# Optimization experiments

Hardware: AMD Instinct MI355X
Metric: run time of the kernel (lower is better)

The kernel has to match this reference:

```python
import jax, jax.numpy as jnp
import numpy as np

H = 64   # hidden_dim
E = 5    # num_edge_features
F = 6    # num_node_features
B, W, N = 8, 12, 200
LN_EPS = 1e-5


def _lstm_layer(x, Wih, Whh, bih, bhh):
    # x: [BN, W, Fin] -> full output sequence [BN, W, H] (PyTorch gate order i,f,g,o)
    BN = x.shape[0]
    h0 = jnp.zeros((BN, Whh.shape[1]), x.dtype)
    def step(carry, xt):
        h, c = carry
        g = xt @ Wih.T + h @ Whh.T + (bih + bhh)
        i, f, gg, o = jnp.split(g, 4, axis=-1)
        c = jax.nn.sigmoid(f) * c + jax.nn.sigmoid(i) * jnp.tanh(gg)
        h = jax.nn.sigmoid(o) * jnp.tanh(c)
        return (h, c), h
    _, ys = jax.lax.scan(step, (h0, h0), jnp.swapaxes(x, 0, 1))
    return jnp.swapaxes(ys, 0, 1)


def _layernorm(x, g, b):
    mu = jnp.mean(x, axis=-1, keepdims=True)
    var = jnp.mean(jnp.square(x - mu), axis=-1, keepdims=True)
    return (x - mu) * jax.lax.rsqrt(var + LN_EPS) * g + b


def setup_inputs() -> dict:
    key = jax.random.key(0)
    ks = jax.random.split(key, 32)
    s = 0.05
    d = {
        'node_features': jax.random.normal(ks[0], (B, W, N, F), jnp.float32),
        'edge_features': jax.random.normal(ks[1], (B, W, N, N, E), jnp.float32),
        'adjacency': jax.random.uniform(ks[2], (B, N, N), jnp.float32),
        # LSTM layer 0 (input F) and layer 1 (input H)
        'Wih0': jax.random.normal(ks[3], (4 * H, F), jnp.float32) * s,
        'Whh0': jax.random.normal(ks[4], (4 * H, H), jnp.float32) * s,
        'bih0': jax.random.normal(ks[5], (4 * H,), jnp.float32) * s,
        'bhh0': jax.random.normal(ks[6], (4 * H,), jnp.float32) * s,
        'Wih1': jax.random.normal(ks[7], (4 * H, H), jnp.float32) * s,
        'Whh1': jax.random.normal(ks[8], (4 * H, H), jnp.float32) * s,
        'bih1': jax.random.normal(ks[9], (4 * H,), jnp.float32) * s,
        'bhh1': jax.random.normal(ks[10], (4 * H,), jnp.float32) * s,
        # 2 GCN layers: linear, edge projection, layernorm
        'gcn_W': jax.random.normal(ks[11], (2, H, H), jnp.float32) * s,
        'gcn_b': jax.random.normal(ks[12], (2, H), jnp.float32) * s,
        'ep_W': jax.random.normal(ks[13], (2, H, E), jnp.float32) * s,
        'ep_b': jax.random.normal(ks[14], (2, H), jnp.float32) * s,
        'ln_g': jnp.ones((2, H), jnp.float32),
        'ln_b': jnp.zeros((2, H), jnp.float32),
        # edge MLP: (2H+E) -> H -> H//2 -> 1
        'mlp_W1': jax.random.normal(ks[15], (H, 2 * H + E), jnp.float32) * s,
        'mlp_b1': jax.random.normal(ks[16], (H,), jnp.float32) * s,
        'mlp_W2': jax.random.normal(ks[17], (H // 2, H), jnp.float32) * s,
        'mlp_b2': jax.random.normal(ks[18], (H // 2,), jnp.float32) * s,
        'mlp_W3': jax.random.normal(ks[19], (1, H // 2), jnp.float32) * s,
        'mlp_b3': jax.random.normal(ks[20], (1,), jnp.float32) * s,
    }
    return d


def reference(node_features, edge_features, adjacency,
              Wih0, Whh0, bih0, bhh0, Wih1, Whh1, bih1, bhh1,
              gcn_W, gcn_b, ep_W, ep_b, ln_g, ln_b,
              mlp_W1, mlp_b1, mlp_W2, mlp_b2, mlp_W3, mlp_b3):
    Bn, Wn, Nn, _ = node_features.shape
    # [B,W,N,F] -> [B*N, W, F]
    x = jnp.transpose(node_features, (0, 2, 1, 3)).reshape(Bn * Nn, Wn, -1)
    y0 = _lstm_layer(x, Wih0, Whh0, bih0, bhh0)      # dropout between layers: eval mode (identity)
    y1 = _lstm_layer(y0, Wih1, Whh1, bih1, bhh1)
    h = y1[:, -1, :].reshape(Bn, Nn, H)

    edge_last = edge_features[:, -1]                 # [B,N,N,E]
    for i in range(2):
        edge_h = edge_last @ ep_W[i].T + ep_b[i]     # [B,N,N,H]
        messages = jnp.einsum('bij,bijn->bin', adjacency, edge_h)
        updated = h @ gcn_W[i].T + gcn_b[i] + messages
        h = jax.nn.relu(_layernorm(updated, ln_g[i], ln_b[i]))
        # dropout: eval mode (identity)

    h_i = jnp.broadcast_to(h[:, :, None, :], (Bn, Nn, Nn, H))
    h_j = jnp.broadcast_to(h[:, None, :, :], (Bn, Nn, Nn, H))
    edge_input = jnp.concatenate([h_i, h_j, edge_last], axis=-1)  # [B,N,N,2H+E]
    z = jax.nn.relu(edge_input @ mlp_W1.T + mlp_b1)
    z = jax.nn.relu(z @ mlp_W2.T + mlp_b2)
    logits = (z @ mlp_W3.T + mlp_b3)[..., 0]
    return jax.nn.sigmoid(logits)
```

## Files before the change

kernel.cpp:

```cpp
#include <hip/hip_runtime.h>
#include <math.h>


#define Hd   64
#define Ed   5
#define Fd   6
#define Bd   8
#define Wd   12
#define Nd   200
#define NSEQ (Bd*Nd)
#define NG   (4*Hd)
#define NEDGE (Bd*Nd*Nd)
#define LNEPS 1e-5f

__device__ __forceinline__ float sigm(float x) { return 1.0f / (1.0f + __expf(-x)); }
__device__ __forceinline__ float tanh_fast(float x) {
  float ax = fabsf(x);
  float t  = __expf(-2.0f * ax);
  float r  = (1.0f - t) / (1.0f + t);
  return copysignf(r, x);
}

__global__ __launch_bounds__(256) void k_prep(
    const float* __restrict__ Wih1, const float* __restrict__ gcn_W,
    const float* __restrict__ ep_W, const float* __restrict__ W1,
    float* __restrict__ Wt1, float* __restrict__ gcnWT,
    float* __restrict__ epWT, float* __restrict__ W1aT,
    float* __restrict__ W1bT)
{
  int idx = blockIdx.x * 256 + threadIdx.x;
  if (idx < 16384) {
    int k = idx >> 8, j = idx & 255;
    Wt1[idx] = Wih1[j * Hd + k];
  } else if (idx < 24576) {
    int r0 = idx - 16384;
    int round = r0 >> 12, rem = r0 & 4095;
    int k = rem >> 6, u = rem & 63;
    gcnWT[r0] = gcn_W[round * 4096 + u * 64 + k];
  } else if (idx < 25216) {
    int r0 = idx - 24576;
    int round = r0 / 320, rem = r0 % 320;
    int e = rem >> 6, u = rem & 63;
    epWT[r0] = ep_W[round * 320 + u * Ed + e];
  } else if (idx < 29312) {
    int r0 = idx - 25216;
    int k = r0 >> 6, n = r0 & 63;
    W1aT[r0] = W1[n * 133 + k];
  } else if (idx < 33408) {
    int r0 = idx - 29312;
    int k = r0 >> 6, n = r0 & 63;
    W1bT[r0] = W1[n * 133 + 64 + k];
  }
}

__global__ __launch_bounds__(256, 3) void k_lstm0(
    const float* __restrict__ nf,
    const float* __restrict__ Wih0, const float* __restrict__ Whh0,
    const float* __restrict__ bih0, const float* __restrict__ bhh0,
    float* __restrict__ y0)
{
  __shared__ float x_sh[Wd * Fd];
  __shared__ float h_sh[Hd];
  __shared__ float gate_sh[2][NG];

  const int tid = threadIdx.x;
  const int seq = blockIdx.x;
  const int b = seq / Nd, n = seq % Nd;
  const int u = tid & 63;

  if (tid < Wd * Fd) {
    int t = tid / Fd, f = tid % Fd;
    x_sh[tid] = nf[((b * Wd + t) * Nd + n) * Fd + f];
  }
  h_sh[u] = 0.f;

  const int j = tid;
  float4 wh[16];
  const float4* wrow = (const float4*)(Whh0 + j * Hd);
  #pragma unroll
  for (int q = 0; q < 16; ++q) wh[q] = wrow[q];
  float wx[Fd];
  #pragma unroll
  for (int f = 0; f < Fd; ++f) wx[f] = Wih0[j * Fd + f];
  const float bias = bih0[j] + bhh0[j];
  const int jt = j >> 6;

  float c = 0.f;
  float yreg[Wd];
  __syncthreads();

  for (int t = 0; t < Wd; ++t) {
    const float* xp = x_sh + t * Fd;
    float a0 = bias, a1 = 0.f, a2 = 0.f, a3 = 0.f;
    #pragma unroll
    for (int f = 0; f < Fd; ++f) a1 += xp[f] * wx[f];
    const float4* h4 = (const float4*)h_sh;
    #pragma unroll
    for (int q = 0; q < 16; ++q) {
      float4 hv = h4[q];
      float d = hv.x * wh[q].x + hv.y * wh[q].y + hv.z * wh[q].z + hv.w * wh[q].w;
      if ((q & 3) == 0) a0 += d; else if ((q & 3) == 1) a1 += d;
      else if ((q & 3) == 2) a2 += d; else a3 += d;
    }
    float acc = (a0 + a1) + (a2 + a3);
    gate_sh[t & 1][j] = (jt == 2) ? tanh_fast(acc) : sigm(acc);
    __syncthreads();
    const float* gb = gate_sh[t & 1];
    float iv = gb[u];
    float fv = gb[64 + u];
    float gv = gb[128 + u];
    float ov = gb[192 + u];
    c = fv * c + iv * gv;
    float h = ov * tanh_fast(c);
    h_sh[u] = h;
    yreg[t] = h;
  }
  if (tid < Hd) {
    #pragma unroll
    for (int t = 0; t < Wd; ++t)
      y0[seq * (Wd * Hd) + t * Hd + u] = yreg[t];
  }
}

__global__ __launch_bounds__(256) void k_xproj1(
    const float* __restrict__ y0,
    const float* __restrict__ Wt1,
    const float* __restrict__ bih1, const float* __restrict__ bhh1,
    float* __restrict__ G1)
{
  __shared__ float ysh[64 * 65];
  __shared__ float osh[2 * 64 * 65];

  const int tid  = threadIdx.x;
  const int row0 = blockIdx.x * 64;
  for (int idx = tid; idx < 64 * 64; idx += 256) {
    int r = idx >> 6, k = idx & 63;
    ysh[r * 65 + k] = y0[(row0 + r) * Hd + k];
  }
  __syncthreads();

  const int w = __builtin_amdgcn_readfirstlane(tid >> 6);
  const int r = tid & 63;
  float acc[64];
  #pragma unroll
  for (int c = 0; c < 64; ++c) acc[c] = 0.f;

  const float* wbase = Wt1 + (w << 6);
  #pragma unroll 2
  for (int k = 0; k < 64; ++k) {
    float yv = ysh[r * 65 + k];
    const float* wk = wbase + k * NG;
    #pragma unroll
    for (int c = 0; c < 64; ++c) acc[c] = fmaf(yv, wk[c], acc[c]);
  }
  #pragma unroll
  for (int c = 0; c < 64; ++c) acc[c] += bih1[(w << 6) + c] + bhh1[(w << 6) + c];

  #pragma unroll
  for (int p = 0; p < 2; ++p) {
    __syncthreads();
    if ((w >> 1) == p) {
      float* orow = osh + ((w & 1) * 64 + r) * 65;
      #pragma unroll
      for (int c = 0; c < 64; ++c) orow[c] = acc[c];
    }
    __syncthreads();
    for (int idx = tid; idx < 2 * 64 * 64; idx += 256) {
      int c  = idx & 127;
      int rr = idx >> 7;
      G1[(row0 + rr) * NG + p * 128 + c] =
          osh[((c >> 6) * 64 + rr) * 65 + (c & 63)];
    }
  }
}

__global__ __launch_bounds__(256, 3) void k_lstm1(
    const float* __restrict__ G1,
    const float* __restrict__ Whh1,
    float* __restrict__ hout)
{
  __shared__ float h_sh[Hd];
  __shared__ float gate_sh[2][NG];

  const int tid = threadIdx.x;
  const int seq = blockIdx.x;
  const int u = tid & 63;
  h_sh[u] = 0.f;

  const int j = tid;
  float4 wh[16];
  const float4* wrow = (const float4*)(Whh1 + j * Hd);
  #pragma unroll
  for (int q = 0; q < 16; ++q) wh[q] = wrow[q];
  const int jt = j >> 6;
  float c = 0.f;
  float hlast = 0.f;

  float g_cur = G1[(seq * Wd + 0) * NG + j];
  __syncthreads();

  for (int t = 0; t < Wd; ++t) {
    float g_next = (t + 1 < Wd) ? G1[(seq * Wd + t + 1) * NG + j] : 0.f;
    float a0 = g_cur;
    float a1 = 0.f, a2 = 0.f, a3 = 0.f;
    const float4* h4 = (const float4*)h_sh;
    #pragma unroll
    for (int q = 0; q < 16; ++q) {
      float4 hv = h4[q];
      float d = hv.x * wh[q].x + hv.y * wh[q].y + hv.z * wh[q].z + hv.w * wh[q].w;
      if ((q & 3) == 0) a0 += d; else if ((q & 3) == 1) a1 += d;
      else if ((q & 3) == 2) a2 += d; else a3 += d;
    }
    float acc = (a0 + a1) + (a2 + a3);
    gate_sh[t & 1][j] = (jt == 2) ? tanh_fast(acc) : sigm(acc);
    __syncthreads();
    const float* gb = gate_sh[t & 1];
    float iv = gb[u];
    float fv = gb[64 + u];
    float gv = gb[128 + u];
    float ov = gb[192 + u];
    c = fv * c + iv * gv;
    float h = ov * tanh_fast(c);
    h_sh[u] = h;
    hlast = h;
    g_cur = g_next;
  }
  if (tid < Hd) hout[seq * Hd + u] = hlast;
}

__global__ __launch_bounds__(256) void k_node(
    const float* __restrict__ ef,    const float* __restrict__ adj,
    const float* __restrict__ h0,
    const float* __restrict__ gcnWT, const float* __restrict__ gcn_b,
    const float* __restrict__ epWT,  const float* __restrict__ ep_b,
    const float* __restrict__ ln_g,  const float* __restrict__ ln_b,
    const float* __restrict__ W1aT,  const float* __restrict__ W1bT,
    const float* __restrict__ b1,
    float* __restrict__ uu, float* __restrict__ vt)
{
  __shared__ float ef_sh[Nd * Ed];
  __shared__ float adj_sh[Nd];
  __shared__ float red[4][6];
  __shared__ float w6[6];
  __shared__ float hcur[Hd];

  const int row = blockIdx.x;
  const int b = row / Nd, i = row % Nd;
  const int tid = threadIdx.x;

  const float* efrow = ef + (size_t)(((b * Wd + (Wd - 1)) * Nd + i)) * (Nd * Ed);
  for (int idx = tid; idx < Nd * Ed; idx += 256) ef_sh[idx] = efrow[idx];
  const float* adjrow = adj + (b * Nd + i) * Nd;
  if (tid < Nd) adj_sh[tid] = adjrow[tid];
  if (tid < Hd) hcur[tid] = h0[row * Hd + tid];
  __syncthreads();

  float p[6] = {0.f, 0.f, 0.f, 0.f, 0.f, 0.f};
  if (tid < Nd) {
    float a = adj_sh[tid];
    p[5] = a;
    #pragma unroll
    for (int k = 0; k < Ed; ++k) p[k] = a * ef_sh[tid * Ed + k];
  }
  #pragma unroll
  for (int k = 0; k < 6; ++k) {
    float v = p[k];
    for (int off = 32; off > 0; off >>= 1) v += __shfl_down(v, off);
    p[k] = v;
  }
  if ((tid & 63) == 0) {
    #pragma unroll
    for (int k = 0; k < 6; ++k) red[tid >> 6][k] = p[k];
  }
  __syncthreads();
  if (tid < 6)
    w6[tid] = red[0][tid] + red[1][tid] + red[2][tid] + red[3][tid];
  __syncthreads();

  const int u = tid & 63;
  #pragma unroll
  for (int round = 0; round < 2; ++round) {
    float hnew = 0.f;
    if (tid < 64) {
      const float* gwT = gcnWT + round * 4096;
      const float* ewT = epWT  + round * 320;
      float acc = gcn_b[round * Hd + u] + w6[5] * ep_b[round * Hd + u];
      #pragma unroll
      for (int e = 0; e < Ed; ++e) acc += w6[e] * ewT[e * 64 + u];
      #pragma unroll 8
      for (int k = 0; k < Hd; ++k) acc += hcur[k] * gwT[k * 64 + u];

      float mu = acc;
      #pragma unroll
      for (int off = 1; off < 64; off <<= 1) mu += __shfl_xor(mu, off);
      mu *= (1.f / 64.f);
      float d = acc - mu;
      float var = d * d;
      #pragma unroll
      for (int off = 1; off < 64; off <<= 1) var += __shfl_xor(var, off);
      var *= (1.f / 64.f);
      float v = d * rsqrtf(var + LNEPS) * ln_g[round * Hd + u] + ln_b[round * Hd + u];
      hnew = fmaxf(v, 0.f);
    }
    __syncthreads();
    if (tid < 64) hcur[tid] = hnew;
    __syncthreads();
  }

  if (tid < 64) {
    float acc = b1[tid];
    #pragma unroll 8
    for (int k = 0; k < Hd; ++k) acc += hcur[k] * W1aT[k * 64 + tid];
    uu[row * Hd + tid] = acc;
  } else if (tid < 128) {
    const int n = tid - 64;
    float acc = 0.f;
    #pragma unroll 8
    for (int k = 0; k < Hd; ++k) acc += hcur[k] * W1bT[k * 64 + n];
    vt[n * NSEQ + row] = acc;
  }
}

__global__ __launch_bounds__(256) void k_mlp(
    const float* __restrict__ ef,
    const float* __restrict__ u, const float* __restrict__ vt,
    const float* __restrict__ W1,
    const float* __restrict__ W2, const float* __restrict__ b2,
    const float* __restrict__ W3, const float* __restrict__ b3,
    float* __restrict__ out)
{
  const int idx = blockIdx.x * 256 + threadIdx.x;
  const int b   = idx / (Nd * Nd);
  const int rem = idx - b * Nd * Nd;
  const int i   = rem / Nd;
  const int jj  = rem - i * Nd;

  const float* e = ef + (((b * Wd + (Wd - 1)) * Nd + i) * Nd + jj) * Ed;
  float e5[Ed];
  #pragma unroll
  for (int q = 0; q < Ed; ++q) e5[q] = e[q];

  const float* ur = u + (b * Nd + i) * Hd;
  const int vcol = b * Nd + jj;

  float z1[64];
  #pragma unroll
  for (int k = 0; k < 64; ++k) {
    float acc = ur[k] + vt[k * NSEQ + vcol];
    const float* w1c = W1 + k * 133 + 128;
    #pragma unroll
    for (int q = 0; q < Ed; ++q) acc += e5[q] * w1c[q];
    z1[k] = fmaxf(acc, 0.f);
  }

  float logit = b3[0];
  #pragma unroll 4
  for (int o = 0; o < 32; ++o) {
    float a0 = b2[o], a1 = 0.f, a2 = 0.f, a3 = 0.f;
    const float* w2 = W2 + o * 64;
    #pragma unroll
    for (int k = 0; k < 64; k += 4) {
      a0 += w2[k]     * z1[k];
      a1 += w2[k + 1] * z1[k + 1];
      a2 += w2[k + 2] * z1[k + 2];
      a3 += w2[k + 3] * z1[k + 3];
    }
    float z2 = fmaxf((a0 + a1) + (a2 + a3), 0.f);
    logit += W3[o] * z2;
  }
  out[idx] = 1.f / (1.f + __expf(-logit));
}

extern "C" void kernel_launch(void* const* d_in, const int* in_sizes, int n_in,
                              void* d_out, int out_size, void* d_ws, size_t ws_size,
                              hipStream_t stream) {
  (void)in_sizes; (void)n_in; (void)out_size; (void)ws_size;
  const float* nf   = (const float*)d_in[0];
  const float* ef   = (const float*)d_in[1];
  const float* adj  = (const float*)d_in[2];
  const float* Wih0 = (const float*)d_in[3];
  const float* Whh0 = (const float*)d_in[4];
  const float* bih0 = (const float*)d_in[5];
  const float* bhh0 = (const float*)d_in[6];
  const float* Wih1 = (const float*)d_in[7];
  const float* Whh1 = (const float*)d_in[8];
  const float* bih1 = (const float*)d_in[9];
  const float* bhh1 = (const float*)d_in[10];
  const float* gcnW = (const float*)d_in[11];
  const float* gcnB = (const float*)d_in[12];
  const float* epW  = (const float*)d_in[13];
  const float* epB  = (const float*)d_in[14];
  const float* lnG  = (const float*)d_in[15];
  const float* lnB  = (const float*)d_in[16];
  const float* W1   = (const float*)d_in[17];
  const float* b1   = (const float*)d_in[18];
  const float* W2   = (const float*)d_in[19];
  const float* b2   = (const float*)d_in[20];
  const float* W3   = (const float*)d_in[21];
  const float* b3   = (const float*)d_in[22];
  float* out = (float*)d_out;

  float* ws   = (float*)d_ws;
  float* y0   = ws;
  float* G1   = y0   + 1228800;
  float* Wt1  = G1   + 4915200;
  float* h0   = Wt1  + 16384;
  float* uu   = h0   + 102400;
  float* vt   = uu   + 102400;
  float* gWT  = vt   + 102400;
  float* eWT  = gWT  + 8192;
  float* W1aT = eWT  + 640;
  float* W1bT = W1aT + 4096;

  k_prep  <<<131,  256, 0, stream>>>(Wih1, gcnW, epW, W1,
                                     Wt1, gWT, eWT, W1aT, W1bT);
  k_lstm0 <<<NSEQ, 256, 0, stream>>>(nf, Wih0, Whh0, bih0, bhh0, y0);
  k_xproj1<<<300,  256, 0, stream>>>(y0, Wt1, bih1, bhh1, G1);
  k_lstm1 <<<NSEQ, 256, 0, stream>>>(G1, Whh1, h0);
  k_node  <<<1600, 256, 0, stream>>>(ef, adj, h0, gWT, gcnB, eWT, epB,
                                     lnG, lnB, W1aT, W1bT, b1, uu, vt);
  k_mlp   <<<1250, 256, 0, stream>>>(ef, uu, vt, W1, W2, b2, W3, b3, out);
}
```

Baseline: 270.2 us.

## Batch four LSTM sequences per block with shared-memory recurrent weights

Replaces the per-sequence LSTM kernels with one generic kernel that processes four sequences per block. The transposed recurrent weights are staged mostly in LDS, with a small tail kept in registers, and each weight load is reused across the four sequences. Layer-0 input projection becomes a separate precompute pass into a G0 buffer, so both layers share the same kernel. This trades an extra 19.6 MB gate buffer write and read, plus a second barrier per step, for less weight traffic and four times fewer blocks.

```diff
diff --git a/kernel.cpp b/kernel.cpp
--- a/kernel.cpp
+++ b/kernel.cpp
@@ -11,6 +11,8 @@
 #define NSEQ (Bd*Nd)
 #define NG   (4*Hd)
 #define NEDGE (Bd*Nd*Nd)
+#define SEQB 4
+#define WROWS 58
 #define LNEPS 1e-5f
 
 __device__ __forceinline__ float sigm(float x) { return 1.0f / (1.0f + __expf(-x)); }
@@ -24,9 +26,14 @@
 __global__ __launch_bounds__(256) void k_prep(
     const float* __restrict__ Wih1, const float* __restrict__ gcn_W,
     const float* __restrict__ ep_W, const float* __restrict__ W1,
+    const float* __restrict__ Wih0, const float* __restrict__ bih0,
+    const float* __restrict__ bhh0, const float* __restrict__ Whh0,
+    const float* __restrict__ Whh1,
     float* __restrict__ Wt1, float* __restrict__ gcnWT,
     float* __restrict__ epWT, float* __restrict__ W1aT,
-    float* __restrict__ W1bT)
+    float* __restrict__ W1bT, float* __restrict__ Wt0,
+    float* __restrict__ b0s, float* __restrict__ WhhT0,
+    float* __restrict__ WhhT1)
 {
   int idx = blockIdx.x * 256 + threadIdx.x;
   if (idx < 16384) {
@@ -50,75 +57,132 @@
     int r0 = idx - 29312;
     int k = r0 >> 6, n = r0 & 63;
     W1bT[r0] = W1[n * 133 + 64 + k];
-  }
-}
-
-__global__ __launch_bounds__(256, 3) void k_lstm0(
-    const float* __restrict__ nf,
-    const float* __restrict__ Wih0, const float* __restrict__ Whh0,
-    const float* __restrict__ bih0, const float* __restrict__ bhh0,
-    float* __restrict__ y0)
-{
-  __shared__ float x_sh[Wd * Fd];
-  __shared__ float h_sh[Hd];
-  __shared__ float gate_sh[2][NG];
-
-  const int tid = threadIdx.x;
-  const int seq = blockIdx.x;
-  const int b = seq / Nd, n = seq % Nd;
-  const int u = tid & 63;
-
-  if (tid < Wd * Fd) {
-    int t = tid / Fd, f = tid % Fd;
-    x_sh[tid] = nf[((b * Wd + t) * Nd + n) * Fd + f];
-  }
-  h_sh[u] = 0.f;
-
-  const int j = tid;
-  float4 wh[16];
-  const float4* wrow = (const float4*)(Whh0 + j * Hd);
-  #pragma unroll
-  for (int q = 0; q < 16; ++q) wh[q] = wrow[q];
-  float wx[Fd];
-  #pragma unroll
-  for (int f = 0; f < Fd; ++f) wx[f] = Wih0[j * Fd + f];
-  const float bias = bih0[j] + bhh0[j];
+  } else if (idx < 34944) {
+    int r0 = idx - 33408;
+    int f = r0 >> 8, j = r0 & 255;
+    Wt0[r0] = Wih0[j * Fd + f];
+  } else if (idx < 35200) {
+    int j = idx - 34944;
+    b0s[j] = bih0[j] + bhh0[j];
+  } else if (idx < 51584) {
+    int r0 = idx - 35200;
+    int k = r0 >> 8, j = r0 & 255;
+    WhhT0[r0] = Whh0[j * Hd + k];
+  } else if (idx < 67968) {
+    int r0 = idx - 51584;
+    int k = r0 >> 8, j = r0 & 255;
+    WhhT1[r0] = Whh1[j * Hd + k];
+  }
+}
+
+__global__ __launch_bounds__(256) void k_xproj0(
+    const float* __restrict__ nf, const float* __restrict__ Wt0,
+    const float* __restrict__ b0s, float* __restrict__ G0)
+{
+  const int j = threadIdx.x;
+  const int row0 = blockIdx.x * 8;
+  float wcol[Fd];
+  #pragma unroll
+  for (int f = 0; f < Fd; ++f) wcol[f] = Wt0[f * NG + j];
+  const float bj = b0s[j];
+  #pragma unroll
+  for (int r = 0; r < 8; ++r) {
+    int row = row0 + r;
+    int seq = row / Wd, t = row % Wd;
+    int b = seq / Nd, n = seq % Nd;
+    const float* xp = nf + ((b * Wd + t) * Nd + n) * Fd;
+    float acc = bj;
+    #pragma unroll
+    for (int f = 0; f < Fd; ++f) acc += xp[f] * wcol[f];
+    G0[row * NG + j] = acc;
+  }
+}
+
+__global__ __launch_bounds__(256, 2) void k_lstm(
+    const float* __restrict__ G,
+    const float* __restrict__ WhhT,
+    float* __restrict__ yfull,
+    float* __restrict__ hlast,
+    int store_all)
+{
+  __shared__ float w_lds[WROWS * NG];
+  __shared__ float h_sh[SEQB][Hd];
+  __shared__ float gate_sh[SEQB][NG];
+
+  const int tid  = threadIdx.x;
+  const int seq0 = blockIdx.x * SEQB;
+  const int j    = tid;
+  const int su   = tid >> 6;
+  const int uu   = tid & 63;
+
+  for (int idx = tid; idx < WROWS * NG; idx += 256) w_lds[idx] = WhhT[idx];
+  float wtail[Hd - WROWS];
+  #pragma unroll
+  for (int q = 0; q < Hd - WROWS; ++q) wtail[q] = WhhT[(WROWS + q) * NG + j];
+  h_sh[su][uu] = 0.f;
+
   const int jt = j >> 6;
-
   float c = 0.f;
   float yreg[Wd];
+  float hl = 0.f;
+
+  float gc[SEQB];
+  #pragma unroll
+  for (int s = 0; s < SEQB; ++s) gc[s] = G[((seq0 + s) * Wd + 0) * NG + j];
   __syncthreads();
 
+#define WK(k) ((k) < WROWS ? w_lds[(k) * NG + j] : wtail[(k) - WROWS])
+
   for (int t = 0; t < Wd; ++t) {
-    const float* xp = x_sh + t * Fd;
-    float a0 = bias, a1 = 0.f, a2 = 0.f, a3 = 0.f;
-    #pragma unroll
-    for (int f = 0; f < Fd; ++f) a1 += xp[f] * wx[f];
-    const float4* h4 = (const float4*)h_sh;
+    float gn[SEQB];
+    #pragma unroll
+    for (int s = 0; s < SEQB; ++s)
+      gn[s] = (t + 1 < Wd) ? G[((seq0 + s) * Wd + t + 1) * NG + j] : 0.f;
+
+    float a[SEQB][4];
+    #pragma unroll
+    for (int s = 0; s < SEQB; ++s) {
+      a[s][0] = gc[s]; a[s][1] = 0.f; a[s][2] = 0.f; a[s][3] = 0.f;
+    }
     #pragma unroll
     for (int q = 0; q < 16; ++q) {
-      float4 hv = h4[q];
-      float d = hv.x * wh[q].x + hv.y * wh[q].y + hv.z * wh[q].z + hv.w * wh[q].w;
-      if ((q & 3) == 0) a0 += d; else if ((q & 3) == 1) a1 += d;
-      else if ((q & 3) == 2) a2 += d; else a3 += d;
-    }
-    float acc = (a0 + a1) + (a2 + a3);
-    gate_sh[t & 1][j] = (jt == 2) ? tanh_fast(acc) : sigm(acc);
-    __syncthreads();
-    const float* gb = gate_sh[t & 1];
-    float iv = gb[u];
-    float fv = gb[64 + u];
-    float gv = gb[128 + u];
-    float ov = gb[192 + u];
-    c = fv * c + iv * gv;
-    float h = ov * tanh_fast(c);
-    h_sh[u] = h;
-    yreg[t] = h;
-  }
-  if (tid < Hd) {
+      float w0 = WK(4 * q), w1 = WK(4 * q + 1);
+      float w2 = WK(4 * q + 2), w3 = WK(4 * q + 3);
+      #pragma unroll
+      for (int s = 0; s < SEQB; ++s) {
+        float4 hv = ((const float4*)h_sh[s])[q];
+        a[s][q & 3] += hv.x * w0 + hv.y * w1 + hv.z * w2 + hv.w * w3;
+      }
+    }
+    #pragma unroll
+    for (int s = 0; s < SEQB; ++s) {
+      float acc = (a[s][0] + a[s][1]) + (a[s][2] + a[s][3]);
+      gate_sh[s][j] = (jt == 2) ? tanh_fast(acc) : sigm(acc);
+    }
+    __syncthreads();
+    {
+      float iv = gate_sh[su][uu];
+      float fv = gate_sh[su][64 + uu];
+      float gv = gate_sh[su][128 + uu];
+      float ov = gate_sh[su][192 + uu];
+      c = fv * c + iv * gv;
+      float h = ov * tanh_fast(c);
+      h_sh[su][uu] = h;
+      yreg[t] = h;
+      hl = h;
+    }
+    __syncthreads();
+    #pragma unroll
+    for (int s = 0; s < SEQB; ++s) gc[s] = gn[s];
+  }
+#undef WK
+
+  if (store_all) {
     #pragma unroll
     for (int t = 0; t < Wd; ++t)
-      y0[seq * (Wd * Hd) + t * Hd + u] = yreg[t];
+      yfull[(seq0 + su) * (Wd * Hd) + t * Hd + uu] = yreg[t];
+  } else {
+    hlast[(seq0 + su) * Hd + uu] = hl;
   }
 }
 
@@ -172,60 +236,6 @@
           osh[((c >> 6) * 64 + rr) * 65 + (c & 63)];
     }
   }
-}
-
-__global__ __launch_bounds__(256, 3) void k_lstm1(
-    const float* __restrict__ G1,
-    const float* __restrict__ Whh1,
-    float* __restrict__ hout)
-{
-  __shared__ float h_sh[Hd];
-  __shared__ float gate_sh[2][NG];
-
-  const int tid = threadIdx.x;
-  const int seq = blockIdx.x;
-  const int u = tid & 63;
-  h_sh[u] = 0.f;
-
-  const int j = tid;
-  float4 wh[16];
-  const float4* wrow = (const float4*)(Whh1 + j * Hd);
-  #pragma unroll
-  for (int q = 0; q < 16; ++q) wh[q] = wrow[q];
-  const int jt = j >> 6;
-  float c = 0.f;
-  float hlast = 0.f;
-
-  float g_cur = G1[(seq * Wd + 0) * NG + j];
-  __syncthreads();
-
-  for (int t = 0; t < Wd; ++t) {
-    float g_next = (t + 1 < Wd) ? G1[(seq * Wd + t + 1) * NG + j] : 0.f;
-    float a0 = g_cur;
-    float a1 = 0.f, a2 = 0.f, a3 = 0.f;
-    const float4* h4 = (const float4*)h_sh;
-    #pragma unroll
-    for (int q = 0; q < 16; ++q) {
-      float4 hv = h4[q];
-      float d = hv.x * wh[q].x + hv.y * wh[q].y + hv.z * wh[q].z + hv.w * wh[q].w;
-      if ((q & 3) == 0) a0 += d; else if ((q & 3) == 1) a1 += d;
-      else if ((q & 3) == 2) a2 += d; else a3 += d;
-    }
-    float acc = (a0 + a1) + (a2 + a3);
-    gate_sh[t & 1][j] = (jt == 2) ? tanh_fast(acc) : sigm(acc);
-    __syncthreads();
-    const float* gb = gate_sh[t & 1];
-    float iv = gb[u];
-    float fv = gb[64 + u];
-    float gv = gb[128 + u];
-    float ov = gb[192 + u];
-    c = fv * c + iv * gv;
-    float h = ov * tanh_fast(c);
-    h_sh[u] = h;
-    hlast = h;
-    g_cur = g_next;
-  }
-  if (tid < Hd) hout[seq * Hd + u] = hlast;
 }
 
 __global__ __launch_bounds__(256) void k_node(
@@ -400,23 +410,30 @@
   const float* b3   = (const float*)d_in[22];
   float* out = (float*)d_out;
 
-  float* ws   = (float*)d_ws;
-  float* y0   = ws;
-  float* G1   = y0   + 1228800;
-  float* Wt1  = G1   + 4915200;
-  float* h0   = Wt1  + 16384;
-  float* uu   = h0   + 102400;
-  float* vt   = uu   + 102400;
-  float* gWT  = vt   + 102400;
-  float* eWT  = gWT  + 8192;
-  float* W1aT = eWT  + 640;
-  float* W1bT = W1aT + 4096;
-
-  k_prep  <<<131,  256, 0, stream>>>(Wih1, gcnW, epW, W1,
-                                     Wt1, gWT, eWT, W1aT, W1bT);
-  k_lstm0 <<<NSEQ, 256, 0, stream>>>(nf, Wih0, Whh0, bih0, bhh0, y0);
+  float* ws    = (float*)d_ws;
+  float* y0    = ws;
+  float* G1    = y0    + 1228800;
+  float* G0    = G1    + 4915200;
+  float* Wt1   = G0    + 4915200;
+  float* h0    = Wt1   + 16384;
+  float* uu    = h0    + 102400;
+  float* vt    = uu    + 102400;
+  float* gWT   = vt    + 102400;
+  float* eWT   = gWT   + 8192;
+  float* W1aT  = eWT   + 640;
+  float* W1bT  = W1aT  + 4096;
+  float* Wt0   = W1bT  + 4096;
+  float* b0s   = Wt0   + 1536;
+  float* WhhT0 = b0s   + 256;
+  float* WhhT1 = WhhT0 + 16384;
+
+  k_prep  <<<266,  256, 0, stream>>>(Wih1, gcnW, epW, W1, Wih0, bih0, bhh0,
+                                     Whh0, Whh1, Wt1, gWT, eWT, W1aT, W1bT,
+                                     Wt0, b0s, WhhT0, WhhT1);
+  k_xproj0<<<2400, 256, 0, stream>>>(nf, Wt0, b0s, G0);
+  k_lstm  <<<NSEQ/SEQB, 256, 0, stream>>>(G0, WhhT0, y0, h0, 1);
   k_xproj1<<<300,  256, 0, stream>>>(y0, Wt1, bih1, bhh1, G1);
-  k_lstm1 <<<NSEQ, 256, 0, stream>>>(G1, Whh1, h0);
+  k_lstm  <<<NSEQ/SEQB, 256, 0, stream>>>(G1, WhhT1, y0, h0, 0);
   k_node  <<<1600, 256, 0, stream>>>(ef, adj, h0, gWT, gcnB, eWT, epB,
                                      lnG, lnB, W1aT, W1bT, b1, uu, vt);
   k_mlp   <<<1250, 256, 0, stream>>>(ef, uu, vt, W1, W2, b2, W3, b3, out);
```

New measurement: 372.9 us. 38.0% more time.

## Fuse layer-1 input projection into LSTM1 and stage recurrent weights in LDS

Applied to the files above, without the earlier changes.

Removes the separate k_xproj1 kernel and its large G1 intermediate buffer by computing each sequence's layer-1 input gates inside k_lstm1 from y0 held in shared memory. Both LSTM kernels now keep most of the transposed recurrent weight matrix (58 of 64 rows) in LDS, plus a small per-thread register tail, instead of 64 floats per thread in registers. The launch-bounds occupancy hint is dropped. The aim is to cut global traffic and register pressure. The cost is about 60KB of LDS per block, which limits blocks per CU, and every block re-reads the weights from global memory.

```diff
diff --git a/kernel.cpp b/kernel.cpp
--- a/kernel.cpp
+++ b/kernel.cpp
@@ -11,6 +11,7 @@
 #define NSEQ (Bd*Nd)
 #define NG   (4*Hd)
 #define NEDGE (Bd*Nd*Nd)
+#define WROWS 58
 #define LNEPS 1e-5f
 
 __device__ __forceinline__ float sigm(float x) { return 1.0f / (1.0f + __expf(-x)); }
@@ -24,9 +25,11 @@
 __global__ __launch_bounds__(256) void k_prep(
     const float* __restrict__ Wih1, const float* __restrict__ gcn_W,
     const float* __restrict__ ep_W, const float* __restrict__ W1,
+    const float* __restrict__ Whh0, const float* __restrict__ Whh1,
     float* __restrict__ Wt1, float* __restrict__ gcnWT,
     float* __restrict__ epWT, float* __restrict__ W1aT,
-    float* __restrict__ W1bT)
+    float* __restrict__ W1bT, float* __restrict__ WhhT0,
+    float* __restrict__ WhhT1)
 {
   int idx = blockIdx.x * 256 + threadIdx.x;
   if (idx < 16384) {
@@ -50,35 +53,46 @@
     int r0 = idx - 29312;
     int k = r0 >> 6, n = r0 & 63;
     W1bT[r0] = W1[n * 133 + 64 + k];
-  }
-}
-
-__global__ __launch_bounds__(256, 3) void k_lstm0(
+  } else if (idx < 49792) {
+    int r0 = idx - 33408;
+    int k = r0 >> 8, j = r0 & 255;
+    WhhT0[r0] = Whh0[j * Hd + k];
+  } else if (idx < 66176) {
+    int r0 = idx - 49792;
+    int k = r0 >> 8, j = r0 & 255;
+    WhhT1[r0] = Whh1[j * Hd + k];
+  }
+}
+
+#define WK(k) ((k) < WROWS ? w_lds[(k) * NG + j] : wtail[(k) - WROWS])
+
+__global__ __launch_bounds__(256) void k_lstm0(
     const float* __restrict__ nf,
-    const float* __restrict__ Wih0, const float* __restrict__ Whh0,
-    const float* __restrict__ bih0, const float* __restrict__ bhh0,
+    const float* __restrict__ Wih0, const float* __restrict__ bih0,
+    const float* __restrict__ bhh0, const float* __restrict__ WhhT0,
     float* __restrict__ y0)
 {
+  __shared__ float w_lds[WROWS * NG];
+  __shared__ float gate_sh[2][NG];
+  __shared__ float h_sh[Hd];
   __shared__ float x_sh[Wd * Fd];
-  __shared__ float h_sh[Hd];
-  __shared__ float gate_sh[2][NG];
 
   const int tid = threadIdx.x;
   const int seq = blockIdx.x;
   const int b = seq / Nd, n = seq % Nd;
   const int u = tid & 63;
-
+  const int j = tid;
+
+  for (int idx = tid; idx < WROWS * NG; idx += 256) w_lds[idx] = WhhT0[idx];
+  float wtail[Hd - WROWS];
+  #pragma unroll
+  for (int q = 0; q < Hd - WROWS; ++q) wtail[q] = WhhT0[(WROWS + q) * NG + j];
   if (tid < Wd * Fd) {
     int t = tid / Fd, f = tid % Fd;
     x_sh[tid] = nf[((b * Wd + t) * Nd + n) * Fd + f];
   }
   h_sh[u] = 0.f;
 
-  const int j = tid;
-  float4 wh[16];
-  const float4* wrow = (const float4*)(Whh0 + j * Hd);
-  #pragma unroll
-  for (int q = 0; q < 16; ++q) wh[q] = wrow[q];
   float wx[Fd];
   #pragma unroll
   for (int f = 0; f < Fd; ++f) wx[f] = Wih0[j * Fd + f];
@@ -89,6 +103,7 @@
   float yreg[Wd];
   __syncthreads();
 
+  #pragma unroll
   for (int t = 0; t < Wd; ++t) {
     const float* xp = x_sh + t * Fd;
     float a0 = bias, a1 = 0.f, a2 = 0.f, a3 = 0.f;
@@ -98,7 +113,9 @@
     #pragma unroll
     for (int q = 0; q < 16; ++q) {
       float4 hv = h4[q];
-      float d = hv.x * wh[q].x + hv.y * wh[q].y + hv.z * wh[q].z + hv.w * wh[q].w;
+      float w0 = WK(4 * q),     w1 = WK(4 * q + 1);
+      float w2 = WK(4 * q + 2), w3 = WK(4 * q + 3);
+      float d = hv.x * w0 + hv.y * w1 + hv.z * w2 + hv.w * w3;
       if ((q & 3) == 0) a0 += d; else if ((q & 3) == 1) a1 += d;
       else if ((q & 3) == 2) a2 += d; else a3 += d;
     }
@@ -122,92 +139,60 @@
   }
 }
 
-__global__ __launch_bounds__(256) void k_xproj1(
+__global__ __launch_bounds__(256) void k_lstm1(
     const float* __restrict__ y0,
     const float* __restrict__ Wt1,
     const float* __restrict__ bih1, const float* __restrict__ bhh1,
-    float* __restrict__ G1)
-{
-  __shared__ float ysh[64 * 65];
-  __shared__ float osh[2 * 64 * 65];
-
-  const int tid  = threadIdx.x;
-  const int row0 = blockIdx.x * 64;
-  for (int idx = tid; idx < 64 * 64; idx += 256) {
-    int r = idx >> 6, k = idx & 63;
-    ysh[r * 65 + k] = y0[(row0 + r) * Hd + k];
-  }
-  __syncthreads();
-
-  const int w = __builtin_amdgcn_readfirstlane(tid >> 6);
-  const int r = tid & 63;
-  float acc[64];
-  #pragma unroll
-  for (int c = 0; c < 64; ++c) acc[c] = 0.f;
-
-  const float* wbase = Wt1 + (w << 6);
-  #pragma unroll 2
-  for (int k = 0; k < 64; ++k) {
-    float yv = ysh[r * 65 + k];
-    const float* wk = wbase + k * NG;
-    #pragma unroll
-    for (int c = 0; c < 64; ++c) acc[c] = fmaf(yv, wk[c], acc[c]);
-  }
-  #pragma unroll
-  for (int c = 0; c < 64; ++c) acc[c] += bih1[(w << 6) + c] + bhh1[(w << 6) + c];
-
-  #pragma unroll
-  for (int p = 0; p < 2; ++p) {
-    __syncthreads();
-    if ((w >> 1) == p) {
-      float* orow = osh + ((w & 1) * 64 + r) * 65;
-      #pragma unroll
-      for (int c = 0; c < 64; ++c) orow[c] = acc[c];
-    }
-    __syncthreads();
-    for (int idx = tid; idx < 2 * 64 * 64; idx += 256) {
-      int c  = idx & 127;
-      int rr = idx >> 7;
-      G1[(row0 + rr) * NG + p * 128 + c] =
-          osh[((c >> 6) * 64 + rr) * 65 + (c & 63)];
-    }
-  }
-}
-
-__global__ __launch_bounds__(256, 3) void k_lstm1(
-    const float* __restrict__ G1,
-    const float* __restrict__ Whh1,
+    const float* __restrict__ WhhT1,
     float* __restrict__ hout)
 {
+  __shared__ float w_lds[WROWS * NG];
+  __shared__ float gate_sh[2][NG];
   __shared__ float h_sh[Hd];
-  __shared__ float gate_sh[2][NG];
+  __shared__ float y0sh[Wd * Hd];
 
   const int tid = threadIdx.x;
   const int seq = blockIdx.x;
   const int u = tid & 63;
+  const int j = tid;
+
+  for (int idx = tid; idx < WROWS * NG; idx += 256) w_lds[idx] = WhhT1[idx];
+  float wtail[Hd - WROWS];
+  #pragma unroll
+  for (int q = 0; q < Hd - WROWS; ++q) wtail[q] = WhhT1[(WROWS + q) * NG + j];
+  for (int idx = tid; idx < Wd * Hd; idx += 256)
+    y0sh[idx] = y0[seq * (Wd * Hd) + idx];
   h_sh[u] = 0.f;
-
-  const int j = tid;
-  float4 wh[16];
-  const float4* wrow = (const float4*)(Whh1 + j * Hd);
-  #pragma unroll
-  for (int q = 0; q < 16; ++q) wh[q] = wrow[q];
+  __syncthreads();
+
+  float g[Wd];
+  #pragma unroll
+  for (int t = 0; t < Wd; ++t) g[t] = 0.f;
+  for (int k = 0; k < Hd; ++k) {
+    float wv = Wt1[k * NG + j];
+    #pragma unroll
+    for (int t = 0; t < Wd; ++t)
+      g[t] = fmaf(y0sh[t * Hd + k], wv, g[t]);
+  }
+  const float bsum = bih1[j] + bhh1[j];
+  #pragma unroll
+  for (int t = 0; t < Wd; ++t) g[t] += bsum;
+
   const int jt = j >> 6;
   float c = 0.f;
   float hlast = 0.f;
 
-  float g_cur = G1[(seq * Wd + 0) * NG + j];
-  __syncthreads();
-
+  #pragma unroll
   for (int t = 0; t < Wd; ++t) {
-    float g_next = (t + 1 < Wd) ? G1[(seq * Wd + t + 1) * NG + j] : 0.f;
-    float a0 = g_cur;
+    float a0 = g[t];
     float a1 = 0.f, a2 = 0.f, a3 = 0.f;
     const float4* h4 = (const float4*)h_sh;
     #pragma unroll
     for (int q = 0; q < 16; ++q) {
       float4 hv = h4[q];
-      float d = hv.x * wh[q].x + hv.y * wh[q].y + hv.z * wh[q].z + hv.w * wh[q].w;
+      float w0 = WK(4 * q),     w1 = WK(4 * q + 1);
+      float w2 = WK(4 * q + 2), w3 = WK(4 * q + 3);
+      float d = hv.x * w0 + hv.y * w1 + hv.z * w2 + hv.w * w3;
       if ((q & 3) == 0) a0 += d; else if ((q & 3) == 1) a1 += d;
       else if ((q & 3) == 2) a2 += d; else a3 += d;
     }
@@ -223,7 +208,6 @@
     float h = ov * tanh_fast(c);
     h_sh[u] = h;
     hlast = h;
-    g_cur = g_next;
   }
   if (tid < Hd) hout[seq * Hd + u] = hlast;
 }
@@ -400,23 +384,23 @@
   const float* b3   = (const float*)d_in[22];
   float* out = (float*)d_out;
 
-  float* ws   = (float*)d_ws;
-  float* y0   = ws;
-  float* G1   = y0   + 1228800;
-  float* Wt1  = G1   + 4915200;
-  float* h0   = Wt1  + 16384;
-  float* uu   = h0   + 102400;
-  float* vt   = uu   + 102400;
-  float* gWT  = vt   + 102400;
-  float* eWT  = gWT  + 8192;
-  float* W1aT = eWT  + 640;
-  float* W1bT = W1aT + 4096;
-
-  k_prep  <<<131,  256, 0, stream>>>(Wih1, gcnW, epW, W1,
-                                     Wt1, gWT, eWT, W1aT, W1bT);
-  k_lstm0 <<<NSEQ, 256, 0, stream>>>(nf, Wih0, Whh0, bih0, bhh0, y0);
-  k_xproj1<<<300,  256, 0, stream>>>(y0, Wt1, bih1, bhh1, G1);
-  k_lstm1 <<<NSEQ, 256, 0, stream>>>(G1, Whh1, h0);
+  float* ws    = (float*)d_ws;
+  float* y0    = ws;
+  float* Wt1   = y0    + 1228800;
+  float* h0    = Wt1   + 16384;
+  float* uu    = h0    + 102400;
+  float* vt    = uu    + 102400;
+  float* gWT   = vt    + 102400;
+  float* eWT   = gWT   + 8192;
+  float* W1aT  = eWT   + 640;
+  float* W1bT  = W1aT  + 4096;
+  float* WhhT0 = W1bT  + 4096;
+  float* WhhT1 = WhhT0 + 16384;
+
+  k_prep  <<<259,  256, 0, stream>>>(Wih1, gcnW, epW, W1, Whh0, Whh1,
+                                     Wt1, gWT, eWT, W1aT, W1bT, WhhT0, WhhT1);
+  k_lstm0 <<<NSEQ, 256, 0, stream>>>(nf, Wih0, bih0, bhh0, WhhT0, y0);
+  k_lstm1 <<<NSEQ, 256, 0, stream>>>(y0, Wt1, bih1, bhh1, WhhT1, h0);
   k_node  <<<1600, 256, 0, stream>>>(ef, adj, h0, gWT, gcnB, eWT, epB,
                                      lnG, lnB, W1aT, W1bT, b1, uu, vt);
   k_mlp   <<<1250, 256, 0, stream>>>(ef, uu, vt, W1, W2, b2, W3, b3, out);
```

After: 304.7 us. +12.8%, slower.

## Process two LSTM sequences per block with LDS weights and readlane broadcast

Applied to the files above, without the earlier changes.

Both LSTM recurrence kernels now handle two sequences per block. The recurrent weight matrix is staged once into padded LDS, where before each thread kept its row in registers. The hidden state is broadcast with readlane from the first wavefront's registers instead of an LDS h buffer, and k_lstm0 writes its outputs through an LDS staging buffer. The goal is to halve the block count, amortize weight loading, and add independent work per sync. In exchange each block uses about 80KB of LDS, occupancy drops to 2 blocks per CU, and every inner-loop step reads weights from LDS.

```diff
diff --git a/kernel.cpp b/kernel.cpp
--- a/kernel.cpp
+++ b/kernel.cpp
@@ -11,6 +11,7 @@
 #define NSEQ (Bd*Nd)
 #define NG   (4*Hd)
 #define NEDGE (Bd*Nd*Nd)
+#define WSTRIDE 68
 #define LNEPS 1e-5f
 
 __device__ __forceinline__ float sigm(float x) { return 1.0f / (1.0f + __expf(-x)); }
@@ -20,13 +21,18 @@
   float r  = (1.0f - t) / (1.0f + t);
   return copysignf(r, x);
 }
+__device__ __forceinline__ float rlane(float v, int lane) {
+  return __uint_as_float(__builtin_amdgcn_readlane(__float_as_uint(v), lane));
+}
 
 __global__ __launch_bounds__(256) void k_prep(
     const float* __restrict__ Wih1, const float* __restrict__ gcn_W,
     const float* __restrict__ ep_W, const float* __restrict__ W1,
+    const float* __restrict__ Whh0, const float* __restrict__ Whh1,
     float* __restrict__ Wt1, float* __restrict__ gcnWT,
     float* __restrict__ epWT, float* __restrict__ W1aT,
-    float* __restrict__ W1bT)
+    float* __restrict__ W1bT, float* __restrict__ Whh0P,
+    float* __restrict__ Whh1P)
 {
   int idx = blockIdx.x * 256 + threadIdx.x;
   if (idx < 16384) {
@@ -50,75 +56,101 @@
     int r0 = idx - 29312;
     int k = r0 >> 6, n = r0 & 63;
     W1bT[r0] = W1[n * 133 + 64 + k];
-  }
-}
-
-__global__ __launch_bounds__(256, 3) void k_lstm0(
+  } else if (idx < 50816) {
+    int r0 = idx - 33408;
+    int j = r0 / WSTRIDE, k = r0 % WSTRIDE;
+    Whh0P[r0] = (k < Hd) ? Whh0[j * Hd + k] : 0.f;
+  } else if (idx < 68224) {
+    int r0 = idx - 50816;
+    int j = r0 / WSTRIDE, k = r0 % WSTRIDE;
+    Whh1P[r0] = (k < Hd) ? Whh1[j * Hd + k] : 0.f;
+  }
+}
+
+__global__ __launch_bounds__(256, 2) void k_lstm0(
     const float* __restrict__ nf,
-    const float* __restrict__ Wih0, const float* __restrict__ Whh0,
-    const float* __restrict__ bih0, const float* __restrict__ bhh0,
+    const float* __restrict__ Wih0, const float* __restrict__ bih0,
+    const float* __restrict__ bhh0, const float* __restrict__ Whh0P,
     float* __restrict__ y0)
 {
-  __shared__ float x_sh[Wd * Fd];
-  __shared__ float h_sh[Hd];
-  __shared__ float gate_sh[2][NG];
-
-  const int tid = threadIdx.x;
-  const int seq = blockIdx.x;
-  const int b = seq / Nd, n = seq % Nd;
+  extern __shared__ float smem[];
+  float* w_lds = smem;
+  float* gates = smem + 17408;
+  float* x_sh  = gates + 1024;
+  float* y_sh  = x_sh + 144;
+
+  const int tid  = threadIdx.x;
+  const int seq0 = blockIdx.x * 2;
+  const int j = tid;
   const int u = tid & 63;
 
-  if (tid < Wd * Fd) {
-    int t = tid / Fd, f = tid % Fd;
-    x_sh[tid] = nf[((b * Wd + t) * Nd + n) * Fd + f];
-  }
-  h_sh[u] = 0.f;
-
-  const int j = tid;
-  float4 wh[16];
-  const float4* wrow = (const float4*)(Whh0 + j * Hd);
-  #pragma unroll
-  for (int q = 0; q < 16; ++q) wh[q] = wrow[q];
+  {
+    const float4* wsrc = (const float4*)Whh0P;
+    float4* wdst = (float4*)w_lds;
+    for (int idx = tid; idx < 4352; idx += 256) wdst[idx] = wsrc[idx];
+  }
+  for (int idx = tid; idx < 2 * Wd * Fd; idx += 256) {
+    int s = idx / (Wd * Fd); int rem = idx % (Wd * Fd);
+    int t = rem / Fd;        int f   = rem % Fd;
+    int seq = seq0 + s; int b = seq / Nd; int n = seq % Nd;
+    x_sh[idx] = nf[((b * Wd + t) * Nd + n) * Fd + f];
+  }
+
   float wx[Fd];
   #pragma unroll
   for (int f = 0; f < Fd; ++f) wx[f] = Wih0[j * Fd + f];
   const float bias = bih0[j] + bhh0[j];
   const int jt = j >> 6;
 
-  float c = 0.f;
-  float yreg[Wd];
-  __syncthreads();
+  float h0v = 0.f, h1v = 0.f, c0 = 0.f, c1 = 0.f;
+  __syncthreads();
+
+  const float4* w4p = (const float4*)w_lds + j * (WSTRIDE / 4);
 
   for (int t = 0; t < Wd; ++t) {
-    const float* xp = x_sh + t * Fd;
-    float a0 = bias, a1 = 0.f, a2 = 0.f, a3 = 0.f;
-    #pragma unroll
-    for (int f = 0; f < Fd; ++f) a1 += xp[f] * wx[f];
-    const float4* h4 = (const float4*)h_sh;
+    const float* xp0 = x_sh + (0 * Wd + t) * Fd;
+    const float* xp1 = x_sh + (1 * Wd + t) * Fd;
+    float as0[4] = {bias, 0.f, 0.f, 0.f};
+    float as1[4] = {bias, 0.f, 0.f, 0.f};
+    #pragma unroll
+    for (int f = 0; f < Fd; ++f) as0[1] += xp0[f] * wx[f];
+    #pragma unroll
+    for (int f = 0; f < Fd; ++f) as1[1] += xp1[f] * wx[f];
     #pragma unroll
     for (int q = 0; q < 16; ++q) {
-      float4 hv = h4[q];
-      float d = hv.x * wh[q].x + hv.y * wh[q].y + hv.z * wh[q].z + hv.w * wh[q].w;
-      if ((q & 3) == 0) a0 += d; else if ((q & 3) == 1) a1 += d;
-      else if ((q & 3) == 2) a2 += d; else a3 += d;
-    }
-    float acc = (a0 + a1) + (a2 + a3);
-    gate_sh[t & 1][j] = (jt == 2) ? tanh_fast(acc) : sigm(acc);
-    __syncthreads();
-    const float* gb = gate_sh[t & 1];
-    float iv = gb[u];
-    float fv = gb[64 + u];
-    float gv = gb[128 + u];
-    float ov = gb[192 + u];
-    c = fv * c + iv * gv;
-    float h = ov * tanh_fast(c);
-    h_sh[u] = h;
-    yreg[t] = h;
-  }
-  if (tid < Hd) {
-    #pragma unroll
-    for (int t = 0; t < Wd; ++t)
-      y0[seq * (Wd * Hd) + t * Hd + u] = yreg[t];
+      float4 w4 = w4p[q];
+      float d0 = rlane(h0v, 4 * q)     * w4.x + rlane(h0v, 4 * q + 1) * w4.y +
+                 rlane(h0v, 4 * q + 2) * w4.z + rlane(h0v, 4 * q + 3) * w4.w;
+      float d1 = rlane(h1v, 4 * q)     * w4.x + rlane(h1v, 4 * q + 1) * w4.y +
+                 rlane(h1v, 4 * q + 2) * w4.z + rlane(h1v, 4 * q + 3) * w4.w;
+      as0[q & 3] += d0;
+      as1[q & 3] += d1;
+    }
+    float acc0 = (as0[0] + as0[1]) + (as0[2] + as0[3]);
+    float acc1 = (as1[0] + as1[1]) + (as1[2] + as1[3]);
+    gates[(t & 1) * 512 + j]       = (jt == 2) ? tanh_fast(acc0) : sigm(acc0);
+    gates[(t & 1) * 512 + 256 + j] = (jt == 2) ? tanh_fast(acc1) : sigm(acc1);
+    __syncthreads();
+    const float* gb = gates + (t & 1) * 512;
+    {
+      float iv = gb[u], fv = gb[64 + u], gv = gb[128 + u], ov = gb[192 + u];
+      c0 = fv * c0 + iv * gv;
+      h0v = ov * tanh_fast(c0);
+    }
+    {
+      float iv = gb[256 + u], fv = gb[320 + u], gv = gb[384 + u], ov = gb[448 + u];
+      c1 = fv * c1 + iv * gv;
+      h1v = ov * tanh_fast(c1);
+    }
+    if (tid < Hd) {
+      y_sh[(0 * Wd + t) * 64 + u] = h0v;
+      y_sh[(1 * Wd + t) * 64 + u] = h1v;
+    }
+  }
+  __syncthreads();
+  for (int idx = tid; idx < 2 * Wd * Hd; idx += 256) {
+    int s = idx / (Wd * Hd), rem = idx % (Wd * Hd);
+    y0[(seq0 + s) * (Wd * Hd) + rem] = y_sh[idx];
   }
 }
 
@@ -174,58 +206,71 @@
   }
 }
 
-__global__ __launch_bounds__(256, 3) void k_lstm1(
+__global__ __launch_bounds__(256, 2) void k_lstm1(
     const float* __restrict__ G1,
-    const float* __restrict__ Whh1,
+    const float* __restrict__ Whh1P,
     float* __restrict__ hout)
 {
-  __shared__ float h_sh[Hd];
-  __shared__ float gate_sh[2][NG];
-
-  const int tid = threadIdx.x;
-  const int seq = blockIdx.x;
+  extern __shared__ float smem[];
+  float* w_lds = smem;
+  float* gates = smem + 17408;
+
+  const int tid  = threadIdx.x;
+  const int seq0 = blockIdx.x * 2;
+  const int j = tid;
   const int u = tid & 63;
-  h_sh[u] = 0.f;
-
-  const int j = tid;
-  float4 wh[16];
-  const float4* wrow = (const float4*)(Whh1 + j * Hd);
-  #pragma unroll
-  for (int q = 0; q < 16; ++q) wh[q] = wrow[q];
+
+  {
+    const float4* wsrc = (const float4*)Whh1P;
+    float4* wdst = (float4*)w_lds;
+    for (int idx = tid; idx < 4352; idx += 256) wdst[idx] = wsrc[idx];
+  }
   const int jt = j >> 6;
-  float c = 0.f;
-  float hlast = 0.f;
-
-  float g_cur = G1[(seq * Wd + 0) * NG + j];
-  __syncthreads();
+  float h0v = 0.f, h1v = 0.f, c0 = 0.f, c1 = 0.f;
+  float gc0 = G1[((seq0 + 0) * Wd + 0) * NG + j];
+  float gc1 = G1[((seq0 + 1) * Wd + 0) * NG + j];
+  __syncthreads();
+
+  const float4* w4p = (const float4*)w_lds + j * (WSTRIDE / 4);
 
   for (int t = 0; t < Wd; ++t) {
-    float g_next = (t + 1 < Wd) ? G1[(seq * Wd + t + 1) * NG + j] : 0.f;
-    float a0 = g_cur;
-    float a1 = 0.f, a2 = 0.f, a3 = 0.f;
-    const float4* h4 = (const float4*)h_sh;
+    float gn0 = (t + 1 < Wd) ? G1[((seq0 + 0) * Wd + t + 1) * NG + j] : 0.f;
+    float gn1 = (t + 1 < Wd) ? G1[((seq0 + 1) * Wd + t + 1) * NG + j] : 0.f;
+    float as0[4] = {gc0, 0.f, 0.f, 0.f};
+    float as1[4] = {gc1, 0.f, 0.f, 0.f};
     #pragma unroll
     for (int q = 0; q < 16; ++q) {
-      float4 hv = h4[q];
-      float d = hv.x * wh[q].x + hv.y * wh[q].y + hv.z * wh[q].z + hv.w * wh[q].w;
-      if ((q & 3) == 0) a0 += d; else if ((q & 3) == 1) a1 += d;
-      else if ((q & 3) == 2) a2 += d; else a3 += d;
-    }
-    float acc = (a0 + a1) + (a2 + a3);
-    gate_sh[t & 1][j] = (jt == 2) ? tanh_fast(acc) : sigm(acc);
-    __syncthreads();
-    const float* gb = gate_sh[t & 1];
-    float iv = gb[u];
-    float fv = gb[64 + u];
-    float gv = gb[128 + u];
-    float ov = gb[192 + u];
-    c = fv * c + iv * gv;
-    float h = ov * tanh_fast(c);
-    h_sh[u] = h;
-    hlast = h;
-    g_cur = g_next;
-  }
-  if (tid < Hd) hout[seq * Hd + u] = hlast;
+      float4 w4 = w4p[q];
+      float d0 = rlane(h0v, 4 * q)     * w4.x + rlane(h0v, 4 * q + 1) * w4.y +
+                 rlane(h0v, 4 * q + 2) * w4.z + rlane(h0v, 4 * q + 3) * w4.w;
+      float d1 = rlane(h1v, 4 * q)     * w4.x + rlane(h1v, 4 * q + 1) * w4.y +
+                 rlane(h1v, 4 * q + 2) * w4.z + rlane(h1v, 4 * q + 3) * w4.w;
+      as0[q & 3] += d0;
+      as1[q & 3] += d1;
+    }
+    float acc0 = (as0[0] + as0[1]) + (as0[2] + as0[3]);
+    float acc1 = (as1[0] + as1[1]) + (as1[2] + as1[3]);
+    gates[(t & 1) * 512 + j]       = (jt == 2) ? tanh_fast(acc0) : sigm(acc0);
+    gates[(t & 1) * 512 + 256 + j] = (jt == 2) ? tanh_fast(acc1) : sigm(acc1);
+    __syncthreads();
+    const float* gb = gates + (t & 1) * 512;
+    {
+      float iv = gb[u], fv = gb[64 + u], gv = gb[128 + u], ov = gb[192 + u];
+      c0 = fv * c0 + iv * gv;
+      h0v = ov * tanh_fast(c0);
+    }
+    {
+      float iv = gb[256 + u], fv = gb[320 + u], gv = gb[384 + u], ov = gb[448 + u];
+      c1 = fv * c1 + iv * gv;
+      h1v = ov * tanh_fast(c1);
+    }
+    gc0 = gn0;
+    gc1 = gn1;
+  }
+  if (tid < 128) {
+    int s = tid >> 6;
+    hout[(seq0 + s) * Hd + u] = (s == 0) ? h0v : h1v;
+  }
 }
 
 __global__ __launch_bounds__(256) void k_node(
@@ -400,23 +445,32 @@
   const float* b3   = (const float*)d_in[22];
   float* out = (float*)d_out;
 
-  float* ws   = (float*)d_ws;
-  float* y0   = ws;
-  float* G1   = y0   + 1228800;
-  float* Wt1  = G1   + 4915200;
-  float* h0   = Wt1  + 16384;
-  float* uu   = h0   + 102400;
-  float* vt   = uu   + 102400;
-  float* gWT  = vt   + 102400;
-  float* eWT  = gWT  + 8192;
-  float* W1aT = eWT  + 640;
-  float* W1bT = W1aT + 4096;
-
-  k_prep  <<<131,  256, 0, stream>>>(Wih1, gcnW, epW, W1,
-                                     Wt1, gWT, eWT, W1aT, W1bT);
-  k_lstm0 <<<NSEQ, 256, 0, stream>>>(nf, Wih0, Whh0, bih0, bhh0, y0);
+  float* ws    = (float*)d_ws;
+  float* y0    = ws;
+  float* G1    = y0    + 1228800;
+  float* Wt1   = G1    + 4915200;
+  float* h0    = Wt1   + 16384;
+  float* uu    = h0    + 102400;
+  float* vt    = uu    + 102400;
+  float* gWT   = vt    + 102400;
+  float* eWT   = gWT   + 8192;
+  float* W1aT  = eWT   + 640;
+  float* W1bT  = W1aT  + 4096;
+  float* Whh0P = W1bT  + 4096;
+  float* Whh1P = Whh0P + 17408;
+
+  const int LDS0 = (17408 + 1024 + 144 + 1536) * 4;
+  const int LDS1 = (17408 + 1024) * 4;
+  hipFuncSetAttribute((const void*)k_lstm0,
+      hipFuncAttributeMaxDynamicSharedMemorySize, LDS0);
+  hipFuncSetAttribute((const void*)k_lstm1,
+      hipFuncAttributeMaxDynamicSharedMemorySize, LDS1);
+
+  k_prep  <<<267,  256, 0, stream>>>(Wih1, gcnW, epW, W1, Whh0, Whh1,
+                                     Wt1, gWT, eWT, W1aT, W1bT, Whh0P, Whh1P);
+  k_lstm0 <<<NSEQ/2, 256, LDS0, stream>>>(nf, Wih0, bih0, bhh0, Whh0P, y0);
   k_xproj1<<<300,  256, 0, stream>>>(y0, Wt1, bih1, bhh1, G1);
-  k_lstm1 <<<NSEQ, 256, 0, stream>>>(G1, Whh1, h0);
+  k_lstm1 <<<NSEQ/2, 256, LDS1, stream>>>(G1, Whh1P, h0);
   k_node  <<<1600, 256, 0, stream>>>(ef, adj, h0, gWT, gcnB, eWT, epB,
                                      lnG, lnB, W1aT, W1bT, b1, uu, vt);
   k_mlp   <<<1250, 256, 0, stream>>>(ef, uu, vt, W1, W2, b2, W3, b3, out);
```

After: 307.2 us. +13.7%, slower.
